# Kernel optimization log

Hardware: AMD Instinct MI355X
Metric: run time of the kernel (lower is better)

## Reference

```python
import jax, jax.numpy as jnp
import numpy as np

NUM_EXPERTS = 8
TOP_K = 2
HIDDEN = 1024
INTER = 4096
LB_WEIGHT = 0.01


def setup_inputs() -> dict:
    key = jax.random.key(0)
    ks = jax.random.split(key, 6)
    s = 0.02
    return {
        "hidden_states": jax.random.normal(ks[0], (2, 2048, HIDDEN), dtype=jnp.float32),
        "Wg": jax.random.normal(ks[1], (HIDDEN, NUM_EXPERTS), dtype=jnp.float32) * s,
        "w1": jax.random.normal(ks[2], (NUM_EXPERTS, HIDDEN, INTER), dtype=jnp.float32) * s,
        "b1": jnp.zeros((NUM_EXPERTS, INTER), dtype=jnp.float32),
        "w2": jax.random.normal(ks[3], (NUM_EXPERTS, INTER, HIDDEN), dtype=jnp.float32) * s,
        "b2": jnp.zeros((NUM_EXPERTS, HIDDEN), dtype=jnp.float32),
    }


def reference(hidden_states, Wg, w1, b1, w2, b2):
    B, S, H = hidden_states.shape
    x = hidden_states.reshape(-1, H)            # [T, H]
    T = x.shape[0]

    # 1. Gating: softmax over experts, top-k selection, renormalized gates
    probs = jax.nn.softmax(x @ Wg, axis=-1)     # [T, E]
    top_v, top_i = jax.lax.top_k(probs, TOP_K)  # [T, K]
    gate = top_v / jnp.sum(top_v, axis=-1, keepdims=True)

    # Load-balancing aux loss: E * sum(frac_assigned * mean_prob) * weight
    frac = jnp.mean(jax.nn.one_hot(top_i, NUM_EXPERTS, dtype=probs.dtype), axis=(0, 1))  # [E]
    mean_p = jnp.mean(probs, axis=0)            # [E]
    aux_loss = NUM_EXPERTS * jnp.sum(frac * mean_p) * LB_WEIGHT

    # Combine weights: per-token weight for each expert (sum of matching top-k gates)
    combine = jnp.zeros((T, NUM_EXPERTS), dtype=x.dtype)
    combine = combine.at[jnp.arange(T)[:, None], top_i].add(gate)  # [T, E]

    # 2-4. Expert FFN + weighted combine (math-equivalent dense-per-expert form)
    out = jnp.zeros_like(x)
    for e in range(NUM_EXPERTS):
        h = jax.nn.gelu(x @ w1[e] + b1[e])       # [T, INTER]
        out = out + combine[:, e:e + 1] * (h @ w2[e] + b2[e])
    return out.reshape(B, S, H), aux_loss
```

## Files before the change

### kernel.cpp

```cpp
#include <hip/hip_runtime.h>
#include <hip/hip_bf16.h>

#define T_TOK   4096
#define HID     1024
#define INTER   4096
#define NEXP    8
#define MAXT    72
#define MAXSLOT 9216
#define TPB_TOK 16

typedef __attribute__((ext_vector_type(8))) short s16x8;
typedef __attribute__((ext_vector_type(4))) float f32x4;

__device__ __forceinline__ void load_lds16(const void* g, void* l) {
    __builtin_amdgcn_global_load_lds(
        (const __attribute__((address_space(1))) void*)g,
        (__attribute__((address_space(3))) void*)l, 16, 0, 0);
}

__device__ __forceinline__ float gelu_tanh(float v) {
    float c = 0.7978845608028654f;
    float u = v + 0.044715f * v * v * v;
    return 0.5f * v * (1.0f + tanhf(c * u));
}

__global__ void transpose_bf16_kernel(const float* __restrict__ in, __hip_bfloat16* __restrict__ out,
                                      int R, int C) {
    __shared__ float tile[32][33];
    size_t eoff = (size_t)blockIdx.z * R * C;
    int c0 = blockIdx.x * 32, r0 = blockIdx.y * 32;
    int tx = threadIdx.x & 31, ty = threadIdx.x >> 5;
    #pragma unroll
    for (int i = 0; i < 32; i += 8)
        tile[ty + i][tx] = in[eoff + (size_t)(r0 + ty + i) * C + c0 + tx];
    __syncthreads();
    #pragma unroll
    for (int i = 0; i < 32; i += 8)
        out[eoff + (size_t)(c0 + ty + i) * R + r0 + tx] = __float2bfloat16(tile[tx][ty + i]);
}

__global__ void gating_kernel(const float* __restrict__ x, const float* __restrict__ Wg,
                              __hip_bfloat16* __restrict__ xb,
                              float* __restrict__ combine, int* __restrict__ counts,
                              float* __restrict__ prob_sums, int* __restrict__ idxcap) {
    __shared__ float s_ps[NEXP];
    __shared__ int   s_cnt[NEXP];
    __shared__ int   s_base[NEXP];
    __shared__ int   s_ei[TPB_TOK][2];
    __shared__ int   s_rk[TPB_TOK][2];

    int tid = threadIdx.x, wv = tid >> 6, ln = tid & 63;
    if (tid < NEXP) { s_ps[tid] = 0.f; s_cnt[tid] = 0; }
    __syncthreads();

    int t0 = blockIdx.x * TPB_TOK;
    for (int sub = 0; sub < 4; ++sub) {
        int tl = wv * 4 + sub;
        int t = t0 + tl;
        const float* xr = x + (size_t)t * HID + ln * 16;
        float4 xv[4];
        #pragma unroll
        for (int i = 0; i < 4; ++i) xv[i] = *(const float4*)(xr + i * 4);

        __hip_bfloat16 row[16];
        #pragma unroll
        for (int i = 0; i < 4; ++i) {
            row[i * 4 + 0] = __float2bfloat16(xv[i].x);
            row[i * 4 + 1] = __float2bfloat16(xv[i].y);
            row[i * 4 + 2] = __float2bfloat16(xv[i].z);
            row[i * 4 + 3] = __float2bfloat16(xv[i].w);
        }
        __hip_bfloat16* xbr = xb + (size_t)t * HID + ln * 16;
        *(s16x8*)(xbr)     = *(s16x8*)&row[0];
        *(s16x8*)(xbr + 8) = *(s16x8*)&row[8];

        float acc[NEXP] = {0,0,0,0,0,0,0,0};
        #pragma unroll
        for (int i = 0; i < 4; ++i) {
            float xs[4] = {xv[i].x, xv[i].y, xv[i].z, xv[i].w};
            #pragma unroll
            for (int j = 0; j < 4; ++j) {
                int k = ln * 16 + i * 4 + j;
                float4 wa = *(const float4*)(Wg + (size_t)k * 8);
                float4 wb = *(const float4*)(Wg + (size_t)k * 8 + 4);
                acc[0] += xs[j] * wa.x; acc[1] += xs[j] * wa.y;
                acc[2] += xs[j] * wa.z; acc[3] += xs[j] * wa.w;
                acc[4] += xs[j] * wb.x; acc[5] += xs[j] * wb.y;
                acc[6] += xs[j] * wb.z; acc[7] += xs[j] * wb.w;
            }
        }
        #pragma unroll
        for (int e = 0; e < NEXP; ++e)
            #pragma unroll
            for (int off = 32; off >= 1; off >>= 1)
                acc[e] += __shfl_xor(acc[e], off);

        float m = acc[0];
        #pragma unroll
        for (int e = 1; e < NEXP; ++e) m = fmaxf(m, acc[e]);
        float p[NEXP], s = 0.f;
        #pragma unroll
        for (int e = 0; e < NEXP; ++e) { p[e] = __expf(acc[e] - m); s += p[e]; }
        float inv = 1.0f / s;
        #pragma unroll
        for (int e = 0; e < NEXP; ++e) p[e] *= inv;

        int i0 = 0;
        #pragma unroll
        for (int e = 1; e < NEXP; ++e) if (p[e] > p[i0]) i0 = e;
        int i1 = (i0 == 0) ? 1 : 0;
        #pragma unroll
        for (int e = 0; e < NEXP; ++e) if (e != i0 && p[e] > p[i1]) i1 = e;
        float gs = p[i0] + p[i1];
        float g0 = p[i0] / gs, g1 = p[i1] / gs;

        if (ln == 0) {
            float rowc[NEXP] = {0,0,0,0,0,0,0,0};
            rowc[i0] = g0; rowc[i1] = g1;
            float4* cr = (float4*)(combine + (size_t)t * NEXP);
            cr[0] = make_float4(rowc[0], rowc[1], rowc[2], rowc[3]);
            cr[1] = make_float4(rowc[4], rowc[5], rowc[6], rowc[7]);
            #pragma unroll
            for (int e = 0; e < NEXP; ++e) atomicAdd(&s_ps[e], p[e]);
            int r0 = atomicAdd(&s_cnt[i0], 1);
            int r1 = atomicAdd(&s_cnt[i1], 1);
            s_ei[tl][0] = i0; s_rk[tl][0] = r0;
            s_ei[tl][1] = i1; s_rk[tl][1] = r1;
        }
    }
    __syncthreads();
    if (tid < NEXP) {
        s_base[tid] = atomicAdd(&counts[tid], s_cnt[tid]);
        atomicAdd(&prob_sums[tid], s_ps[tid]);
    }
    __syncthreads();
    if (tid < TPB_TOK * 2) {
        int tl = tid >> 1, k = tid & 1;
        int e = s_ei[tl][k];
        idxcap[e * T_TOK + s_base[e] + s_rk[tl][k]] = t0 + tl;
    }
}

__global__ void plan_kernel(const int* __restrict__ counts, const float* __restrict__ prob_sums,
                            int* __restrict__ offs, int* __restrict__ tile_e,
                            int* __restrict__ tile_s0, int* __restrict__ tile_nv,
                            int* __restrict__ ntiles, float* __restrict__ aux_out) {
    int tt = 0, o = 0;
    for (int e = 0; e < NEXP; ++e) {
        offs[e] = o;
        int n = counts[e];
        int nt = (n + 127) >> 7;
        for (int r = 0; r < nt; ++r) {
            tile_e[tt] = e;
            tile_s0[tt] = o + r * 128;
            int nv = n - r * 128; if (nv > 128) nv = 128;
            tile_nv[tt] = nv;
            ++tt;
        }
        o += nt * 128;
    }
    *ntiles = tt;
    float aux = 0.f;
    for (int e = 0; e < NEXP; ++e)
        aux += ((float)counts[e] / (float)(T_TOK * 2)) * (prob_sums[e] / (float)T_TOK);
    aux_out[0] = (float)NEXP * aux * 0.01f;
}

__global__ void compact_kernel(const int* __restrict__ counts, const int* __restrict__ offs,
                               const int* __restrict__ tile_e, const int* __restrict__ tile_s0,
                               const int* __restrict__ ntiles,
                               const int* __restrict__ idxcap, int* __restrict__ idxc) {
    int tt = blockIdx.x;
    if (tt >= *ntiles) return;
    int e = tile_e[tt];
    int slot = tile_s0[tt] + threadIdx.x;
    int i = slot - offs[e];
    int n = counts[e];
    idxc[slot] = (i < n) ? idxcap[e * T_TOK + i] : 0;
}


__global__ __launch_bounds__(256, 2)
void gemm1_kernel(const __hip_bfloat16* __restrict__ xb,
                  const __hip_bfloat16* __restrict__ w1b,
                  const float* __restrict__ b1,
                  const int* __restrict__ idxc,
                  const int* __restrict__ tile_e, const int* __restrict__ tile_s0,
                  const int* __restrict__ ntiles,
                  __hip_bfloat16* __restrict__ h)
{
    const int NWG = MAXT * (INTER / 128);
    int bid = blockIdx.x;
    int w = (bid & 7) * (NWG / 8) + (bid >> 3);
    int tt = w >> 5;
    int n0 = (w & 31) * 128;
    if (tt >= *ntiles) return;
    int e = tile_e[tt];
    int slot0 = tile_s0[tt];

    __shared__ __hip_bfloat16 As[2][128][64];
    __shared__ __hip_bfloat16 Bs[2][128][64];
    __shared__ int s_idx[128];

    int tid = threadIdx.x, wv = tid >> 6, ln = tid & 63;
    if (tid < 128) s_idx[tid] = idxc[slot0 + tid];
    __syncthreads();

    int swz = ((ln & 7) ^ (ln >> 3)) * 8;
    const __hip_bfloat16* srcA[4];
    const __hip_bfloat16* srcB[4];
    const __hip_bfloat16* wbase = w1b + (size_t)e * INTER * HID;
    #pragma unroll
    for (int j = 0; j < 4; ++j) {
        int r = wv * 32 + j * 8 + (ln >> 3);
        srcA[j] = xb + (size_t)s_idx[r] * HID + swz;
        srcB[j] = wbase + (size_t)(n0 + r) * HID + swz;
    }

    f32x4 acc[4][4] = {};
    int wr = wv >> 1, wc = wv & 1, lr = ln & 15;

    auto STAGE = [&](int b, int kt) {
        #pragma unroll
        for (int j = 0; j < 4; ++j) {
            load_lds16(srcA[j] + kt, (void*)&As[b][wv * 32 + j * 8][0]);
            load_lds16(srcB[j] + kt, (void*)&Bs[b][wv * 32 + j * 8][0]);
        }
    };
    auto COMPUTE = [&](int b) {
        #pragma unroll
        for (int kk = 0; kk < 2; ++kk) {
            int lslot = (((kk * 4) + (ln >> 4)) ^ (ln & 7)) * 16;
            s16x8 af[4], bf[4];
            #pragma unroll
            for (int m = 0; m < 4; ++m) {
                int row = wr * 64 + m * 16 + lr;
                af[m] = *(const s16x8*)((const char*)&As[b][0][0] + row * 128 + lslot);
            }
            #pragma unroll
            for (int n = 0; n < 4; ++n) {
                int row = wc * 64 + n * 16 + lr;
                bf[n] = *(const s16x8*)((const char*)&Bs[b][0][0] + row * 128 + lslot);
            }
            #pragma unroll
            for (int m = 0; m < 4; ++m)
                #pragma unroll
                for (int n = 0; n < 4; ++n)
                    acc[m][n] = __builtin_amdgcn_mfma_f32_16x16x32_bf16(af[m], bf[n], acc[m][n], 0, 0, 0);
        }
    };

    STAGE(0, 0);
    __syncthreads();
    int cur = 0;
    const int NT = HID / 64;
    for (int t = 0; t < NT; ++t) {
        if (t + 1 < NT) STAGE(cur ^ 1, (t + 1) * 64);
        COMPUTE(cur);
        __syncthreads();
        cur ^= 1;
    }

    const float* b1e = b1 + (size_t)e * INTER;
    int rq = (ln >> 4) * 4;
    #pragma unroll
    for (int m = 0; m < 4; ++m) {
        #pragma unroll
        for (int r = 0; r < 4; ++r) {
            int row = wr * 64 + m * 16 + rq + r;
            size_t hrow = (size_t)(slot0 + row) * INTER;
            #pragma unroll
            for (int n = 0; n < 4; ++n) {
                int col = n0 + wc * 64 + n * 16 + lr;
                float v = acc[m][n][r] + b1e[col];
                h[hrow + col] = __float2bfloat16(gelu_tanh(v));
            }
        }
    }
}

__global__ __launch_bounds__(256, 2)
void gemm2_kernel(const __hip_bfloat16* __restrict__ h,
                  const __hip_bfloat16* __restrict__ w2b,
                  const float* __restrict__ b2,
                  const float* __restrict__ combine,
                  const int* __restrict__ idxc,
                  const int* __restrict__ tile_e, const int* __restrict__ tile_s0,
                  const int* __restrict__ tile_nv, const int* __restrict__ ntiles,
                  float* __restrict__ out)
{
    const int NWG = MAXT * (HID / 128);
    int bid = blockIdx.x;
    int w = (bid & 7) * (NWG / 8) + (bid >> 3);
    int tt = w >> 3;
    int n0 = (w & 7) * 128;
    if (tt >= *ntiles) return;
    int e = tile_e[tt];
    int slot0 = tile_s0[tt];

    __shared__ __hip_bfloat16 As[2][128][64];
    __shared__ __hip_bfloat16 Bs[2][128][64];
    __shared__ int s_idx[128];

    int tid = threadIdx.x, wv = tid >> 6, ln = tid & 63;
    if (tid < 128) s_idx[tid] = idxc[slot0 + tid];

    int swz = ((ln & 7) ^ (ln >> 3)) * 8;
    const __hip_bfloat16* srcA[4];
    const __hip_bfloat16* srcB[4];
    const __hip_bfloat16* wbase = w2b + (size_t)e * HID * INTER;
    #pragma unroll
    for (int j = 0; j < 4; ++j) {
        int r = wv * 32 + j * 8 + (ln >> 3);
        srcA[j] = h + (size_t)(slot0 + r) * INTER + swz;
        srcB[j] = wbase + (size_t)(n0 + r) * INTER + swz;
    }

    f32x4 acc[4][4] = {};
    int wr = wv >> 1, wc = wv & 1, lr = ln & 15;

    auto STAGE = [&](int b, int kt) {
        #pragma unroll
        for (int j = 0; j < 4; ++j) {
            load_lds16(srcA[j] + kt, (void*)&As[b][wv * 32 + j * 8][0]);
            load_lds16(srcB[j] + kt, (void*)&Bs[b][wv * 32 + j * 8][0]);
        }
    };
    auto COMPUTE = [&](int b) {
        #pragma unroll
        for (int kk = 0; kk < 2; ++kk) {
            int lslot = (((kk * 4) + (ln >> 4)) ^ (ln & 7)) * 16;
            s16x8 af[4], bf[4];
            #pragma unroll
            for (int m = 0; m < 4; ++m) {
                int row = wr * 64 + m * 16 + lr;
                af[m] = *(const s16x8*)((const char*)&As[b][0][0] + row * 128 + lslot);
            }
            #pragma unroll
            for (int n = 0; n < 4; ++n) {
                int row = wc * 64 + n * 16 + lr;
                bf[n] = *(const s16x8*)((const char*)&Bs[b][0][0] + row * 128 + lslot);
            }
            #pragma unroll
            for (int m = 0; m < 4; ++m)
                #pragma unroll
                for (int n = 0; n < 4; ++n)
                    acc[m][n] = __builtin_amdgcn_mfma_f32_16x16x32_bf16(af[m], bf[n], acc[m][n], 0, 0, 0);
        }
    };

    STAGE(0, 0);
    __syncthreads();
    int cur = 0;
    const int NT = INTER / 64;
    for (int t = 0; t < NT; ++t) {
        if (t + 1 < NT) STAGE(cur ^ 1, (t + 1) * 64);
        COMPUTE(cur);
        __syncthreads();
        cur ^= 1;
    }

    const float* b2e = b2 + (size_t)e * HID;
    int nv = tile_nv[tt];
    int rq = (ln >> 4) * 4;
    #pragma unroll
    for (int m = 0; m < 4; ++m) {
        #pragma unroll
        for (int r = 0; r < 4; ++r) {
            int row = wr * 64 + m * 16 + rq + r;
            if (row < nv) {
                int tok = s_idx[row];
                float g = combine[(size_t)tok * 8 + e];
                #pragma unroll
                for (int n = 0; n < 4; ++n) {
                    int col = n0 + wc * 64 + n * 16 + lr;
                    float v = acc[m][n][r] + b2e[col];
                    atomicAdd(&out[(size_t)tok * HID + col], g * v);
                }
            }
        }
    }
}

static const size_t OFF_XB      = 0;
static const size_t SZ_XB       = (size_t)T_TOK * HID * 2;
static const size_t OFF_W1B     = OFF_XB + SZ_XB;
static const size_t SZ_W        = (size_t)NEXP * INTER * HID * 2;
static const size_t OFF_W2B     = OFF_W1B + SZ_W;
static const size_t OFF_H       = OFF_W2B + SZ_W;
static const size_t SZ_H        = (size_t)MAXSLOT * INTER * 2;
static const size_t OFF_COMBINE = OFF_H + SZ_H;
static const size_t OFF_IDXCAP  = OFF_COMBINE + (size_t)T_TOK * 8 * 4;
static const size_t OFF_IDXC    = OFF_IDXCAP + (size_t)NEXP * T_TOK * 4;
static const size_t OFF_COUNTS  = OFF_IDXC + (size_t)MAXSLOT * 4;
static const size_t OFF_PSUMS   = OFF_COUNTS + 32;
static const size_t OFF_OFFS    = OFF_PSUMS + 32;
static const size_t OFF_TILE_E  = OFF_OFFS + 64;
static const size_t OFF_TILE_S0 = OFF_TILE_E + 512;
static const size_t OFF_TILE_NV = OFF_TILE_S0 + 512;
static const size_t OFF_NTILES  = OFF_TILE_NV + 512;

extern "C" void kernel_launch(void* const* d_in, const int* in_sizes, int n_in,
                              void* d_out, int out_size, void* d_ws, size_t ws_size,
                              hipStream_t stream) {
    const float* x  = (const float*)d_in[0];
    const float* Wg = (const float*)d_in[1];
    const float* w1 = (const float*)d_in[2];
    const float* b1 = (const float*)d_in[3];
    const float* w2 = (const float*)d_in[4];
    const float* b2 = (const float*)d_in[5];
    float* out = (float*)d_out;
    char* ws = (char*)d_ws;

    __hip_bfloat16* xb   = (__hip_bfloat16*)(ws + OFF_XB);
    __hip_bfloat16* w1b  = (__hip_bfloat16*)(ws + OFF_W1B);
    __hip_bfloat16* w2b  = (__hip_bfloat16*)(ws + OFF_W2B);
    __hip_bfloat16* h    = (__hip_bfloat16*)(ws + OFF_H);
    float* combine       = (float*)(ws + OFF_COMBINE);
    int*   idxcap        = (int*)(ws + OFF_IDXCAP);
    int*   idxc          = (int*)(ws + OFF_IDXC);
    int*   counts        = (int*)(ws + OFF_COUNTS);
    float* psums         = (float*)(ws + OFF_PSUMS);
    int*   offs          = (int*)(ws + OFF_OFFS);
    int*   tile_e        = (int*)(ws + OFF_TILE_E);
    int*   tile_s0       = (int*)(ws + OFF_TILE_S0);
    int*   tile_nv       = (int*)(ws + OFF_TILE_NV);
    int*   ntiles        = (int*)(ws + OFF_NTILES);

    (void)hipMemsetAsync(out, 0, (size_t)out_size * sizeof(float), stream);
    (void)hipMemsetAsync(ws + OFF_COUNTS, 0, 64, stream);

    transpose_bf16_kernel<<<dim3(INTER / 32, HID / 32, NEXP), 256, 0, stream>>>(w1, w1b, HID, INTER);
    transpose_bf16_kernel<<<dim3(HID / 32, INTER / 32, NEXP), 256, 0, stream>>>(w2, w2b, INTER, HID);
    gating_kernel<<<T_TOK / TPB_TOK, 256, 0, stream>>>(x, Wg, xb, combine, counts, psums, idxcap);
    plan_kernel<<<1, 1, 0, stream>>>(counts, psums, offs, tile_e, tile_s0, tile_nv, ntiles,
                                     out + (size_t)T_TOK * HID);
    compact_kernel<<<MAXT, 128, 0, stream>>>(counts, offs, tile_e, tile_s0, ntiles, idxcap, idxc);
    gemm1_kernel<<<MAXT * (INTER / 128), 256, 0, stream>>>(xb, w1b, b1, idxc, tile_e, tile_s0,
                                                           ntiles, h);
    gemm2_kernel<<<MAXT * (HID / 128), 256, 0, stream>>>(h, w2b, b2, combine, idxc, tile_e,
                                                         tile_s0, tile_nv, ntiles, out);
}
```

Measured before the change: 462.3 us.

## Split gemm2 along K into two halves and drop LDS double buffering

Both expert GEMMs drop their double-buffered LDS staging and use a single buffer, with a barrier before and after each compute step. The second GEMM is also split along its K dimension into two halves, which doubles the number of workgroups. Each half adds its partial sums into the output atomically, and only the first half adds the bias. The aim is more parallelism for the smaller second GEMM and lower LDS use, at the cost of losing load/compute overlap and doubling the atomic traffic to the output.

After: 382.8 us. 17.2% less time.

```diff
diff --git a/kernel.cpp b/kernel.cpp
--- a/kernel.cpp
+++ b/kernel.cpp
@@ -198,8 +198,8 @@
     int e = tile_e[tt];
     int slot0 = tile_s0[tt];
 
-    __shared__ __hip_bfloat16 As[2][128][64];
-    __shared__ __hip_bfloat16 Bs[2][128][64];
+    __shared__ __hip_bfloat16 As[128][64];
+    __shared__ __hip_bfloat16 Bs[128][64];
     __shared__ int s_idx[128];
 
     int tid = threadIdx.x, wv = tid >> 6, ln = tid & 63;
@@ -220,14 +220,13 @@
     f32x4 acc[4][4] = {};
     int wr = wv >> 1, wc = wv & 1, lr = ln & 15;
 
-    auto STAGE = [&](int b, int kt) {
+    for (int kt = 0; kt < HID; kt += 64) {
         #pragma unroll
         for (int j = 0; j < 4; ++j) {
-            load_lds16(srcA[j] + kt, (void*)&As[b][wv * 32 + j * 8][0]);
-            load_lds16(srcB[j] + kt, (void*)&Bs[b][wv * 32 + j * 8][0]);
-        }
-    };
-    auto COMPUTE = [&](int b) {
+            load_lds16(srcA[j] + kt, (void*)&As[wv * 32 + j * 8][0]);
+            load_lds16(srcB[j] + kt, (void*)&Bs[wv * 32 + j * 8][0]);
+        }
+        __syncthreads();
         #pragma unroll
         for (int kk = 0; kk < 2; ++kk) {
             int lslot = (((kk * 4) + (ln >> 4)) ^ (ln & 7)) * 16;
@@ -235,12 +234,12 @@
             #pragma unroll
             for (int m = 0; m < 4; ++m) {
                 int row = wr * 64 + m * 16 + lr;
-                af[m] = *(const s16x8*)((const char*)&As[b][0][0] + row * 128 + lslot);
+                af[m] = *(const s16x8*)((const char*)&As[0][0] + row * 128 + lslot);
             }
             #pragma unroll
             for (int n = 0; n < 4; ++n) {
                 int row = wc * 64 + n * 16 + lr;
-                bf[n] = *(const s16x8*)((const char*)&Bs[b][0][0] + row * 128 + lslot);
+                bf[n] = *(const s16x8*)((const char*)&Bs[0][0] + row * 128 + lslot);
             }
             #pragma unroll
             for (int m = 0; m < 4; ++m)
@@ -248,17 +247,7 @@
                 for (int n = 0; n < 4; ++n)
                     acc[m][n] = __builtin_amdgcn_mfma_f32_16x16x32_bf16(af[m], bf[n], acc[m][n], 0, 0, 0);
         }
-    };
-
-    STAGE(0, 0);
-    __syncthreads();
-    int cur = 0;
-    const int NT = HID / 64;
-    for (int t = 0; t < NT; ++t) {
-        if (t + 1 < NT) STAGE(cur ^ 1, (t + 1) * 64);
-        COMPUTE(cur);
         __syncthreads();
-        cur ^= 1;
     }
 
     const float* b1e = b1 + (size_t)e * INTER;
@@ -289,17 +278,18 @@
                   const int* __restrict__ tile_nv, const int* __restrict__ ntiles,
                   float* __restrict__ out)
 {
-    const int NWG = MAXT * (HID / 128);
+    const int NWG = MAXT * (HID / 128) * 2;
     int bid = blockIdx.x;
     int w = (bid & 7) * (NWG / 8) + (bid >> 3);
-    int tt = w >> 3;
-    int n0 = (w & 7) * 128;
+    int ks = w & 1;
+    int n0 = ((w >> 1) & 7) * 128;
+    int tt = w >> 4;
     if (tt >= *ntiles) return;
     int e = tile_e[tt];
     int slot0 = tile_s0[tt];
 
-    __shared__ __hip_bfloat16 As[2][128][64];
-    __shared__ __hip_bfloat16 Bs[2][128][64];
+    __shared__ __hip_bfloat16 As[128][64];
+    __shared__ __hip_bfloat16 Bs[128][64];
     __shared__ int s_idx[128];
 
     int tid = threadIdx.x, wv = tid >> 6, ln = tid & 63;
@@ -319,14 +309,14 @@
     f32x4 acc[4][4] = {};
     int wr = wv >> 1, wc = wv & 1, lr = ln & 15;
 
-    auto STAGE = [&](int b, int kt) {
+    int k0 = ks * (INTER / 2), k1 = k0 + INTER / 2;
+    for (int kt = k0; kt < k1; kt += 64) {
         #pragma unroll
         for (int j = 0; j < 4; ++j) {
-            load_lds16(srcA[j] + kt, (void*)&As[b][wv * 32 + j * 8][0]);
-            load_lds16(srcB[j] + kt, (void*)&Bs[b][wv * 32 + j * 8][0]);
-        }
-    };
-    auto COMPUTE = [&](int b) {
+            load_lds16(srcA[j] + kt, (void*)&As[wv * 32 + j * 8][0]);
+            load_lds16(srcB[j] + kt, (void*)&Bs[wv * 32 + j * 8][0]);
+        }
+        __syncthreads();
         #pragma unroll
         for (int kk = 0; kk < 2; ++kk) {
             int lslot = (((kk * 4) + (ln >> 4)) ^ (ln & 7)) * 16;
@@ -334,12 +324,12 @@
             #pragma unroll
             for (int m = 0; m < 4; ++m) {
                 int row = wr * 64 + m * 16 + lr;
-                af[m] = *(const s16x8*)((const char*)&As[b][0][0] + row * 128 + lslot);
+                af[m] = *(const s16x8*)((const char*)&As[0][0] + row * 128 + lslot);
             }
             #pragma unroll
             for (int n = 0; n < 4; ++n) {
                 int row = wc * 64 + n * 16 + lr;
-                bf[n] = *(const s16x8*)((const char*)&Bs[b][0][0] + row * 128 + lslot);
+                bf[n] = *(const s16x8*)((const char*)&Bs[0][0] + row * 128 + lslot);
             }
             #pragma unroll
             for (int m = 0; m < 4; ++m)
@@ -347,17 +337,7 @@
                 for (int n = 0; n < 4; ++n)
                     acc[m][n] = __builtin_amdgcn_mfma_f32_16x16x32_bf16(af[m], bf[n], acc[m][n], 0, 0, 0);
         }
-    };
-
-    STAGE(0, 0);
-    __syncthreads();
-    int cur = 0;
-    const int NT = INTER / 64;
-    for (int t = 0; t < NT; ++t) {
-        if (t + 1 < NT) STAGE(cur ^ 1, (t + 1) * 64);
-        COMPUTE(cur);
         __syncthreads();
-        cur ^= 1;
     }
 
     const float* b2e = b2 + (size_t)e * HID;
@@ -374,7 +354,7 @@
                 #pragma unroll
                 for (int n = 0; n < 4; ++n) {
                     int col = n0 + wc * 64 + n * 16 + lr;
-                    float v = acc[m][n][r] + b2e[col];
+                    float v = acc[m][n][r] + (ks == 0 ? b2e[col] : 0.f);
                     atomicAdd(&out[(size_t)tok * HID + col], g * v);
                 }
             }
@@ -438,6 +418,6 @@
     compact_kernel<<<MAXT, 128, 0, stream>>>(counts, offs, tile_e, tile_s0, ntiles, idxcap, idxc);
     gemm1_kernel<<<MAXT * (INTER / 128), 256, 0, stream>>>(xb, w1b, b1, idxc, tile_e, tile_s0,
                                                            ntiles, h);
-    gemm2_kernel<<<MAXT * (HID / 128), 256, 0, stream>>>(h, w2b, b2, combine, idxc, tile_e,
-                                                         tile_s0, tile_nv, ntiles, out);
-}
+    gemm2_kernel<<<MAXT * (HID / 128) * 2, 256, 0, stream>>>(h, w2b, b2, combine, idxc, tile_e,
+                                                             tile_s0, tile_nv, ntiles, out);
+}
```
